# Kernel optimization log

Measured on AMD Instinct MI355X. Metric: run time of the kernel, lower is better.

Reference implementation:

```python
import jax, jax.numpy as jnp
import numpy as np

T, H, I = 4096, 4096, 11008  # tokens, hidden, intermediate


def setup_inputs() -> dict:
    key = jax.random.key(0)
    k = jax.random.split(key, 6)
    # int8-range quantized activations and weights (stored as int32 for jax matmul)
    x_q = jax.random.randint(k[0], (T, H), -127, 128).astype(jnp.int32)
    w_gate_up = jax.random.randint(k[1], (2 * I, H), -127, 128).astype(jnp.int32)
    w_down = jax.random.randint(k[2], (H, I), -127, 128).astype(jnp.int32)
    # per-token dynamic input scale, per-output-channel weight scales
    x_scale = jax.random.uniform(k[3], (T,), jnp.float32, 1e-4, 2e-2)
    s_w_gate_up = jax.random.uniform(k[4], (2 * I,), jnp.float32, 1e-4, 2e-2)
    s_w_down = jax.random.uniform(k[5], (H,), jnp.float32, 1e-4, 2e-2)
    return {"x_q": x_q, "x_scale": x_scale, "w_gate_up": w_gate_up,
            "s_w_gate_up": s_w_gate_up, "w_down": w_down, "s_w_down": s_w_down}


def reference(x_q, x_scale, w_gate_up, s_w_gate_up, w_down, s_w_down):
    # --- gate_up_proj: W8A8 int8 GEMM + dequant (per-token x per-channel scales) ---
    gu_i32 = jnp.matmul(x_q, w_gate_up.T)                                   # [T, 2I] int32 accum
    gu = gu_i32.astype(jnp.float32) * x_scale[:, None] * s_w_gate_up[None, :]
    gate, up = gu[:, :I], gu[:, I:]
    # --- SiluAndMulQuant: fused SiLU(gate)*up + per-token dynamic requant to int8 ---
    y = jax.nn.silu(gate) * up                                              # [T, I] fp
    s2 = jnp.maximum(jnp.max(jnp.abs(y), axis=-1), 1e-8) / 127.0            # [T] new dynamic scale
    y_q = jnp.clip(jnp.round(y / s2[:, None]), -128.0, 127.0).astype(jnp.int32)
    # --- down_proj: W8A8 int8 GEMM + dequant ---
    out_i32 = jnp.matmul(y_q, w_down.T)                                     # [T, H] int32 accum
    out = out_i32.astype(jnp.float32) * s2[:, None] * s_w_down[None, :]
    return out
```

## Files before the change

### kernel.cpp

```cpp
#include <hip/hip_runtime.h>
#include <cstdint>
#include <cstddef>

#define T_DIM 4096
#define H_DIM 4096
#define I_DIM 11008

typedef int v4i __attribute__((ext_vector_type(4)));

__device__ __forceinline__ void async_copy16(const void* g, void* l) {
  __builtin_amdgcn_global_load_lds(
      (const __attribute__((address_space(1))) void*)g,
      (__attribute__((address_space(3))) void*)l, 16, 0, 0);
}

__device__ __forceinline__ void stage_tile(const int8_t* src, size_t ld,
                                           char* ldsbase, int wave, int lane) {
#pragma unroll
  for (int q = 0; q < 2; ++q) {
    int seg = q * 4 + wave;
    int r = seg * 16 + (lane >> 2);
    int p = lane & 3;
    int c = p ^ ((r >> 1) & 3);
    const int8_t* g = src + (size_t)r * ld + (size_t)c * 16;
    char* lp = ldsbase + seg * 1024;
    async_copy16((const void*)g, (void*)lp);
  }
}

__device__ __forceinline__ v4i frag_load(const char* ldsbase, int rowbase, int lane) {
  int r = rowbase + (lane & 15);
  int c = (lane >> 4) ^ ((r >> 1) & 3);
  return *(const v4i*)(ldsbase + r * 64 + c * 16);
}

__global__ void pack_i8(const int4* __restrict__ src, char4* __restrict__ dst, int n4) {
  int stride = gridDim.x * blockDim.x;
  for (int i = blockIdx.x * blockDim.x + threadIdx.x; i < n4; i += stride) {
    int4 v = src[i];
    char4 c;
    c.x = (char)v.x; c.y = (char)v.y; c.z = (char)v.z; c.w = (char)v.w;
    dst[i] = c;
  }
}

__global__ void zero_u32(unsigned* __restrict__ p, int n) {
  int i = blockIdx.x * blockDim.x + threadIdx.x;
  if (i < n) p[i] = 0u;
}

__global__ __launch_bounds__(256, 2)
void gemm1_silu(const int8_t* __restrict__ x8,
                const int8_t* __restrict__ wgu8,
                const float* __restrict__ x_scale,
                const float* __restrict__ s_wgu,
                float* __restrict__ y,
                unsigned* __restrict__ rowmax) {
  __shared__ __align__(16) char lds[24 * 1024];
  char* ldsA  = lds;
  char* ldsBg = lds + 8192;
  char* ldsBu = lds + 16384;

  const int tid = threadIdx.x;
  const int wave = tid >> 6, lane = tid & 63;
  const int wm = wave >> 1, wn = wave & 1;
  const int m0 = blockIdx.y * 128;
  const int n0 = blockIdx.x * 128;

  v4i accg[4][4], accu[4][4];
  const v4i vzero = {0, 0, 0, 0};
#pragma unroll
  for (int i = 0; i < 4; i++)
#pragma unroll
    for (int j = 0; j < 4; j++) { accg[i][j] = vzero; accu[i][j] = vzero; }

  const int8_t* Ab  = x8 + (size_t)m0 * H_DIM;
  const int8_t* Bgb = wgu8 + (size_t)n0 * H_DIM;
  const int8_t* Bub = wgu8 + ((size_t)I_DIM + (size_t)n0) * H_DIM;

  for (int k0 = 0; k0 < H_DIM; k0 += 64) {
    __syncthreads();
    stage_tile(Ab + k0, H_DIM, ldsA, wave, lane);
    stage_tile(Bgb + k0, H_DIM, ldsBg, wave, lane);
    stage_tile(Bub + k0, H_DIM, ldsBu, wave, lane);
    __syncthreads();

    v4i a[4], bg[4], bu[4];
#pragma unroll
    for (int i = 0; i < 4; i++) a[i]  = frag_load(ldsA,  wm * 64 + i * 16, lane);
#pragma unroll
    for (int j = 0; j < 4; j++) bg[j] = frag_load(ldsBg, wn * 64 + j * 16, lane);
#pragma unroll
    for (int j = 0; j < 4; j++) bu[j] = frag_load(ldsBu, wn * 64 + j * 16, lane);

#pragma unroll
    for (int i = 0; i < 4; i++)
#pragma unroll
      for (int j = 0; j < 4; j++) {
        accg[i][j] = __builtin_amdgcn_mfma_i32_16x16x64_i8(a[i], bg[j], accg[i][j], 0, 0, 0);
        accu[i][j] = __builtin_amdgcn_mfma_i32_16x16x64_i8(a[i], bu[j], accu[i][j], 0, 0, 0);
      }
  }

  const int lr = lane >> 4;
  const int lc = lane & 15;
#pragma unroll
  for (int i = 0; i < 4; i++) {
#pragma unroll
    for (int t = 0; t < 4; t++) {
      const int gr = m0 + wm * 64 + i * 16 + lr * 4 + t;
      const float sx = x_scale[gr];
      float vmax = 0.f;
#pragma unroll
      for (int j = 0; j < 4; j++) {
        const int gc = n0 + wn * 64 + j * 16 + lc;
        float g = (float)accg[i][j][t] * sx * s_wgu[gc];
        float u = (float)accu[i][j][t] * sx * s_wgu[I_DIM + gc];
        float yv = (g / (1.f + expf(-g))) * u;
        y[(size_t)gr * I_DIM + gc] = yv;
        vmax = fmaxf(vmax, fabsf(yv));
      }
#pragma unroll
      for (int off = 1; off < 16; off <<= 1)
        vmax = fmaxf(vmax, __shfl_xor(vmax, off, 64));
      if (lc == 0) atomicMax(&rowmax[gr], __float_as_uint(vmax));
    }
  }
}

__global__ void quantize_y(const float* __restrict__ y,
                           const unsigned* __restrict__ rowmax,
                           int8_t* __restrict__ yq) {
  size_t gid = (size_t)blockIdx.x * blockDim.x + threadIdx.x;
  size_t base = gid * 4;
  if (base >= (size_t)T_DIM * I_DIM) return;
  int row = (int)(base / I_DIM);
  float inv = 127.f / fmaxf(__uint_as_float(rowmax[row]), 1e-8f);
  float4 v = *(const float4*)(y + base);
  char4 q;
  q.x = (char)(int)fminf(127.f, fmaxf(-128.f, rintf(v.x * inv)));
  q.y = (char)(int)fminf(127.f, fmaxf(-128.f, rintf(v.y * inv)));
  q.z = (char)(int)fminf(127.f, fmaxf(-128.f, rintf(v.z * inv)));
  q.w = (char)(int)fminf(127.f, fmaxf(-128.f, rintf(v.w * inv)));
  *(char4*)(yq + base) = q;
}

__global__ __launch_bounds__(256, 2)
void gemm2_scaled(const int8_t* __restrict__ yq8,
                  const int8_t* __restrict__ wd8,
                  const unsigned* __restrict__ rowmax,
                  const float* __restrict__ s_wd,
                  float* __restrict__ out) {
  __shared__ __align__(16) char lds[16 * 1024];
  char* ldsA = lds;
  char* ldsB = lds + 8192;

  const int tid = threadIdx.x;
  const int wave = tid >> 6, lane = tid & 63;
  const int wm = wave >> 1, wn = wave & 1;
  const int m0 = blockIdx.y * 128;
  const int n0 = blockIdx.x * 128;

  v4i acc[4][4];
  const v4i vzero = {0, 0, 0, 0};
#pragma unroll
  for (int i = 0; i < 4; i++)
#pragma unroll
    for (int j = 0; j < 4; j++) acc[i][j] = vzero;

  const int8_t* Ab = yq8 + (size_t)m0 * I_DIM;
  const int8_t* Bb = wd8 + (size_t)n0 * I_DIM;

  for (int k0 = 0; k0 < I_DIM; k0 += 64) {
    __syncthreads();
    stage_tile(Ab + k0, I_DIM, ldsA, wave, lane);
    stage_tile(Bb + k0, I_DIM, ldsB, wave, lane);
    __syncthreads();

    v4i a[4], b[4];
#pragma unroll
    for (int i = 0; i < 4; i++) a[i] = frag_load(ldsA, wm * 64 + i * 16, lane);
#pragma unroll
    for (int j = 0; j < 4; j++) b[j] = frag_load(ldsB, wn * 64 + j * 16, lane);

#pragma unroll
    for (int i = 0; i < 4; i++)
#pragma unroll
      for (int j = 0; j < 4; j++)
        acc[i][j] = __builtin_amdgcn_mfma_i32_16x16x64_i8(a[i], b[j], acc[i][j], 0, 0, 0);
  }

  const int lr = lane >> 4;
  const int lc = lane & 15;
#pragma unroll
  for (int i = 0; i < 4; i++) {
#pragma unroll
    for (int t = 0; t < 4; t++) {
      const int gr = m0 + wm * 64 + i * 16 + lr * 4 + t;
      const float s2 = fmaxf(__uint_as_float(rowmax[gr]), 1e-8f) / 127.f;
#pragma unroll
      for (int j = 0; j < 4; j++) {
        const int gc = n0 + wn * 64 + j * 16 + lc;
        out[(size_t)gr * H_DIM + gc] = (float)acc[i][j][t] * s2 * s_wd[gc];
      }
    }
  }
}

extern "C" void kernel_launch(void* const* d_in, const int* in_sizes, int n_in,
                              void* d_out, int out_size, void* d_ws, size_t ws_size,
                              hipStream_t stream) {
  const int*   x_q     = (const int*)d_in[0];
  const float* x_scale = (const float*)d_in[1];
  const int*   w_gu    = (const int*)d_in[2];
  const float* s_wgu   = (const float*)d_in[3];
  const int*   w_d     = (const int*)d_in[4];
  const float* s_wd    = (const float*)d_in[5];
  float* out = (float*)d_out;

  char* ws = (char*)d_ws;
  const size_t SZ_X8   = (size_t)T_DIM * H_DIM;
  const size_t SZ_WGU8 = (size_t)2 * I_DIM * H_DIM;
  const size_t SZ_WD8  = (size_t)H_DIM * I_DIM;
  const size_t SZ_Y    = (size_t)T_DIM * I_DIM * 4;
  const size_t SZ_YQ   = (size_t)T_DIM * I_DIM;

  int8_t*   x8     = (int8_t*)ws;
  int8_t*   wgu8   = (int8_t*)(ws + SZ_X8);
  int8_t*   wd8    = (int8_t*)(ws + SZ_X8 + SZ_WGU8);
  float*    y      = (float*)(ws + SZ_X8 + SZ_WGU8 + SZ_WD8);
  int8_t*   yq8    = (int8_t*)(ws + SZ_X8 + SZ_WGU8 + SZ_WD8 + SZ_Y);
  unsigned* rowmax = (unsigned*)(ws + SZ_X8 + SZ_WGU8 + SZ_WD8 + SZ_Y + SZ_YQ);

  pack_i8<<<dim3(8192), dim3(256), 0, stream>>>((const int4*)x_q,  (char4*)x8,   (int)(SZ_X8 / 4));
  pack_i8<<<dim3(8192), dim3(256), 0, stream>>>((const int4*)w_gu, (char4*)wgu8, (int)(SZ_WGU8 / 4));
  pack_i8<<<dim3(8192), dim3(256), 0, stream>>>((const int4*)w_d,  (char4*)wd8,  (int)(SZ_WD8 / 4));
  zero_u32<<<dim3(16), dim3(256), 0, stream>>>(rowmax, T_DIM);

  gemm1_silu<<<dim3(I_DIM / 128, T_DIM / 128), dim3(256), 0, stream>>>(
      x8, wgu8, x_scale, s_wgu, y, rowmax);

  quantize_y<<<dim3((unsigned)((size_t)T_DIM * I_DIM / 4 / 256)), dim3(256), 0, stream>>>(
      y, rowmax, yq8);

  gemm2_scaled<<<dim3(H_DIM / 128, T_DIM / 128), dim3(256), 0, stream>>>(
      yq8, wd8, rowmax, s_wd, out);
}
```

Baseline: 1.488 ms.

## Double-buffer LDS tiles and swizzle workgroup order in both int8 GEMMs

Both GEMM kernels now stage the next K tile into a second LDS buffer while MFMAs run on the current one. This removes one barrier per K step and overlaps global-to-LDS async copies with compute. Workgroup IDs are remapped with a stride-8 swizzle so that consecutive tiles land on the same XCD, which is meant to improve L2 reuse of A and B tiles. gemm2's launch bound also rises to 3 blocks per SIMD hint. In exchange, LDS use per block doubles, which could limit occupancy.

```diff
diff --git a/kernel.cpp b/kernel.cpp
--- a/kernel.cpp
+++ b/kernel.cpp
@@ -49,6 +49,25 @@
   if (i < n) p[i] = 0u;
 }
 
+__device__ __forceinline__ void g1_step(const char* LA, const char* LBG, const char* LBU,
+                                        int wm, int wn, int lane,
+                                        v4i (&accg)[4][4], v4i (&accu)[4][4]) {
+  v4i a[4], bg[4], bu[4];
+#pragma unroll
+  for (int i = 0; i < 4; i++) a[i]  = frag_load(LA,  wm * 64 + i * 16, lane);
+#pragma unroll
+  for (int j = 0; j < 4; j++) bg[j] = frag_load(LBG, wn * 64 + j * 16, lane);
+#pragma unroll
+  for (int j = 0; j < 4; j++) bu[j] = frag_load(LBU, wn * 64 + j * 16, lane);
+#pragma unroll
+  for (int i = 0; i < 4; i++)
+#pragma unroll
+    for (int j = 0; j < 4; j++) {
+      accg[i][j] = __builtin_amdgcn_mfma_i32_16x16x64_i8(a[i], bg[j], accg[i][j], 0, 0, 0);
+      accu[i][j] = __builtin_amdgcn_mfma_i32_16x16x64_i8(a[i], bu[j], accu[i][j], 0, 0, 0);
+    }
+}
+
 __global__ __launch_bounds__(256, 2)
 void gemm1_silu(const int8_t* __restrict__ x8,
                 const int8_t* __restrict__ wgu8,
@@ -56,16 +75,21 @@
                 const float* __restrict__ s_wgu,
                 float* __restrict__ y,
                 unsigned* __restrict__ rowmax) {
-  __shared__ __align__(16) char lds[24 * 1024];
-  char* ldsA  = lds;
-  char* ldsBg = lds + 8192;
-  char* ldsBu = lds + 16384;
+  __shared__ __align__(16) char lds0[24576];
+  __shared__ __align__(16) char lds1[24576];
+  char* A0 = lds0;  char* Bg0 = lds0 + 8192;  char* Bu0 = lds0 + 16384;
+  char* A1 = lds1;  char* Bg1 = lds1 + 8192;  char* Bu1 = lds1 + 16384;
 
   const int tid = threadIdx.x;
   const int wave = tid >> 6, lane = tid & 63;
   const int wm = wave >> 1, wn = wave & 1;
-  const int m0 = blockIdx.y * 128;
-  const int n0 = blockIdx.x * 128;
+
+  const unsigned nwg = gridDim.x * gridDim.y;
+  const unsigned bid = blockIdx.y * gridDim.x + blockIdx.x;
+  const unsigned cpx = nwg >> 3;
+  const unsigned swz = (bid & 7) * cpx + (bid >> 3);
+  const int m0 = (int)(swz / gridDim.x) * 128;
+  const int n0 = (int)(swz % gridDim.x) * 128;
 
   v4i accg[4][4], accu[4][4];
   const v4i vzero = {0, 0, 0, 0};
@@ -78,28 +102,32 @@
   const int8_t* Bgb = wgu8 + (size_t)n0 * H_DIM;
   const int8_t* Bub = wgu8 + ((size_t)I_DIM + (size_t)n0) * H_DIM;
 
-  for (int k0 = 0; k0 < H_DIM; k0 += 64) {
-    __syncthreads();
-    stage_tile(Ab + k0, H_DIM, ldsA, wave, lane);
-    stage_tile(Bgb + k0, H_DIM, ldsBg, wave, lane);
-    stage_tile(Bub + k0, H_DIM, ldsBu, wave, lane);
-    __syncthreads();
-
-    v4i a[4], bg[4], bu[4];
-#pragma unroll
-    for (int i = 0; i < 4; i++) a[i]  = frag_load(ldsA,  wm * 64 + i * 16, lane);
-#pragma unroll
-    for (int j = 0; j < 4; j++) bg[j] = frag_load(ldsBg, wn * 64 + j * 16, lane);
-#pragma unroll
-    for (int j = 0; j < 4; j++) bu[j] = frag_load(ldsBu, wn * 64 + j * 16, lane);
-
-#pragma unroll
-    for (int i = 0; i < 4; i++)
-#pragma unroll
-      for (int j = 0; j < 4; j++) {
-        accg[i][j] = __builtin_amdgcn_mfma_i32_16x16x64_i8(a[i], bg[j], accg[i][j], 0, 0, 0);
-        accu[i][j] = __builtin_amdgcn_mfma_i32_16x16x64_i8(a[i], bu[j], accu[i][j], 0, 0, 0);
-      }
+  stage_tile(Ab,  H_DIM, A0,  wave, lane);
+  stage_tile(Bgb, H_DIM, Bg0, wave, lane);
+  stage_tile(Bub, H_DIM, Bu0, wave, lane);
+  __syncthreads();
+
+  for (int k0 = 0; k0 < H_DIM; k0 += 128) {
+    {
+      const int kn = k0 + 64;
+      if (kn < H_DIM) {
+        stage_tile(Ab + kn,  H_DIM, A1,  wave, lane);
+        stage_tile(Bgb + kn, H_DIM, Bg1, wave, lane);
+        stage_tile(Bub + kn, H_DIM, Bu1, wave, lane);
+      }
+      g1_step(A0, Bg0, Bu0, wm, wn, lane, accg, accu);
+      __syncthreads();
+    }
+    {
+      const int kn = k0 + 128;
+      if (kn < H_DIM) {
+        stage_tile(Ab + kn,  H_DIM, A0,  wave, lane);
+        stage_tile(Bgb + kn, H_DIM, Bg0, wave, lane);
+        stage_tile(Bub + kn, H_DIM, Bu0, wave, lane);
+      }
+      g1_step(A1, Bg1, Bu1, wm, wn, lane, accg, accu);
+      __syncthreads();
+    }
   }
 
   const int lr = lane >> 4;
@@ -145,21 +173,42 @@
   *(char4*)(yq + base) = q;
 }
 
-__global__ __launch_bounds__(256, 2)
+__device__ __forceinline__ void g2_step(const char* LA, const char* LB,
+                                        int wm, int wn, int lane,
+                                        v4i (&acc)[4][4]) {
+  v4i a[4], b[4];
+#pragma unroll
+  for (int i = 0; i < 4; i++) a[i] = frag_load(LA, wm * 64 + i * 16, lane);
+#pragma unroll
+  for (int j = 0; j < 4; j++) b[j] = frag_load(LB, wn * 64 + j * 16, lane);
+#pragma unroll
+  for (int i = 0; i < 4; i++)
+#pragma unroll
+    for (int j = 0; j < 4; j++)
+      acc[i][j] = __builtin_amdgcn_mfma_i32_16x16x64_i8(a[i], b[j], acc[i][j], 0, 0, 0);
+}
+
+__global__ __launch_bounds__(256, 3)
 void gemm2_scaled(const int8_t* __restrict__ yq8,
                   const int8_t* __restrict__ wd8,
                   const unsigned* __restrict__ rowmax,
                   const float* __restrict__ s_wd,
                   float* __restrict__ out) {
-  __shared__ __align__(16) char lds[16 * 1024];
-  char* ldsA = lds;
-  char* ldsB = lds + 8192;
+  __shared__ __align__(16) char lds0[16384];
+  __shared__ __align__(16) char lds1[16384];
+  char* A0 = lds0;  char* B0 = lds0 + 8192;
+  char* A1 = lds1;  char* B1 = lds1 + 8192;
 
   const int tid = threadIdx.x;
   const int wave = tid >> 6, lane = tid & 63;
   const int wm = wave >> 1, wn = wave & 1;
-  const int m0 = blockIdx.y * 128;
-  const int n0 = blockIdx.x * 128;
+
+  const unsigned nwg = gridDim.x * gridDim.y;
+  const unsigned bid = blockIdx.y * gridDim.x + blockIdx.x;
+  const unsigned cpx = nwg >> 3;
+  const unsigned swz = (bid & 7) * cpx + (bid >> 3);
+  const int m0 = (int)(swz / gridDim.x) * 128;
+  const int n0 = (int)(swz % gridDim.x) * 128;
 
   v4i acc[4][4];
   const v4i vzero = {0, 0, 0, 0};
@@ -171,23 +220,29 @@
   const int8_t* Ab = yq8 + (size_t)m0 * I_DIM;
   const int8_t* Bb = wd8 + (size_t)n0 * I_DIM;
 
-  for (int k0 = 0; k0 < I_DIM; k0 += 64) {
-    __syncthreads();
-    stage_tile(Ab + k0, I_DIM, ldsA, wave, lane);
-    stage_tile(Bb + k0, I_DIM, ldsB, wave, lane);
-    __syncthreads();
-
-    v4i a[4], b[4];
-#pragma unroll
-    for (int i = 0; i < 4; i++) a[i] = frag_load(ldsA, wm * 64 + i * 16, lane);
-#pragma unroll
-    for (int j = 0; j < 4; j++) b[j] = frag_load(ldsB, wn * 64 + j * 16, lane);
-
-#pragma unroll
-    for (int i = 0; i < 4; i++)
-#pragma unroll
-      for (int j = 0; j < 4; j++)
-        acc[i][j] = __builtin_amdgcn_mfma_i32_16x16x64_i8(a[i], b[j], acc[i][j], 0, 0, 0);
+  stage_tile(Ab, I_DIM, A0, wave, lane);
+  stage_tile(Bb, I_DIM, B0, wave, lane);
+  __syncthreads();
+
+  for (int k0 = 0; k0 < I_DIM; k0 += 128) {
+    {
+      const int kn = k0 + 64;
+      if (kn < I_DIM) {
+        stage_tile(Ab + kn, I_DIM, A1, wave, lane);
+        stage_tile(Bb + kn, I_DIM, B1, wave, lane);
+      }
+      g2_step(A0, B0, wm, wn, lane, acc);
+      __syncthreads();
+    }
+    {
+      const int kn = k0 + 128;
+      if (kn < I_DIM) {
+        stage_tile(Ab + kn, I_DIM, A0, wave, lane);
+        stage_tile(Bb + kn, I_DIM, B0, wave, lane);
+      }
+      g2_step(A1, B1, wm, wn, lane, acc);
+      __syncthreads();
+    }
   }
 
   const int lr = lane >> 4;
```

Measured after the change: 1.475 ms. About the same (-0.8%).

## Triple-buffer LDS with async prefetch and XCD-aware tile swizzle in both GEMMs

Applied to the files above, without the earlier changes.

Both int8 GEMMs now use three LDS buffers, prefetching tiles two K-steps ahead with global_load_lds. Each step uses one vmcnt wait and one barrier instead of two __syncthreads, so global loads overlap MFMA work. Block indices are remapped so blocks that land on the same XCD share A rows, which should improve L2 reuse. LDS per block triples and gemm2 raises its occupancy hint to 3. The hand-counted vmcnt values and the unguarded final step depend on exact tile counts (64 and 172).

```diff
diff --git a/kernel.cpp b/kernel.cpp
--- a/kernel.cpp
+++ b/kernel.cpp
@@ -12,26 +12,6 @@
   __builtin_amdgcn_global_load_lds(
       (const __attribute__((address_space(1))) void*)g,
       (__attribute__((address_space(3))) void*)l, 16, 0, 0);
-}
-
-__device__ __forceinline__ void stage_tile(const int8_t* src, size_t ld,
-                                           char* ldsbase, int wave, int lane) {
-#pragma unroll
-  for (int q = 0; q < 2; ++q) {
-    int seg = q * 4 + wave;
-    int r = seg * 16 + (lane >> 2);
-    int p = lane & 3;
-    int c = p ^ ((r >> 1) & 3);
-    const int8_t* g = src + (size_t)r * ld + (size_t)c * 16;
-    char* lp = ldsbase + seg * 1024;
-    async_copy16((const void*)g, (void*)lp);
-  }
-}
-
-__device__ __forceinline__ v4i frag_load(const char* ldsbase, int rowbase, int lane) {
-  int r = rowbase + (lane & 15);
-  int c = (lane >> 4) ^ ((r >> 1) & 3);
-  return *(const v4i*)(ldsbase + r * 64 + c * 16);
 }
 
 __global__ void pack_i8(const int4* __restrict__ src, char4* __restrict__ dst, int n4) {
@@ -56,16 +36,21 @@
                 const float* __restrict__ s_wgu,
                 float* __restrict__ y,
                 unsigned* __restrict__ rowmax) {
-  __shared__ __align__(16) char lds[24 * 1024];
-  char* ldsA  = lds;
-  char* ldsBg = lds + 8192;
-  char* ldsBu = lds + 16384;
+  __shared__ __align__(16) char lds0[24576];
+  __shared__ __align__(16) char lds1[24576];
+  __shared__ __align__(16) char lds2[24576];
 
   const int tid = threadIdx.x;
   const int wave = tid >> 6, lane = tid & 63;
   const int wm = wave >> 1, wn = wave & 1;
-  const int m0 = blockIdx.y * 128;
-  const int n0 = blockIdx.x * 128;
+
+  const unsigned bid = blockIdx.y * gridDim.x + blockIdx.x;
+  const unsigned xcd = bid & 7;
+  const unsigned l   = bid >> 3;
+  const unsigned s   = l >> 5;
+  const unsigned r   = l - (s << 5);
+  const int m0 = (int)(xcd * 4 + (r & 3)) * 128;
+  const int n0 = (int)(s * 8 + (r >> 2)) * 128;
 
   v4i accg[4][4], accu[4][4];
   const v4i vzero = {0, 0, 0, 0};
@@ -78,29 +63,72 @@
   const int8_t* Bgb = wgu8 + (size_t)n0 * H_DIM;
   const int8_t* Bub = wgu8 + ((size_t)I_DIM + (size_t)n0) * H_DIM;
 
-  for (int k0 = 0; k0 < H_DIM; k0 += 64) {
-    __syncthreads();
-    stage_tile(Ab + k0, H_DIM, ldsA, wave, lane);
-    stage_tile(Bgb + k0, H_DIM, ldsBg, wave, lane);
-    stage_tile(Bub + k0, H_DIM, ldsBu, wave, lane);
-    __syncthreads();
-
-    v4i a[4], bg[4], bu[4];
-#pragma unroll
-    for (int i = 0; i < 4; i++) a[i]  = frag_load(ldsA,  wm * 64 + i * 16, lane);
-#pragma unroll
-    for (int j = 0; j < 4; j++) bg[j] = frag_load(ldsBg, wn * 64 + j * 16, lane);
-#pragma unroll
-    for (int j = 0; j < 4; j++) bu[j] = frag_load(ldsBu, wn * 64 + j * 16, lane);
-
-#pragma unroll
-    for (int i = 0; i < 4; i++)
-#pragma unroll
-      for (int j = 0; j < 4; j++) {
-        accg[i][j] = __builtin_amdgcn_mfma_i32_16x16x64_i8(a[i], bg[j], accg[i][j], 0, 0, 0);
-        accu[i][j] = __builtin_amdgcn_mfma_i32_16x16x64_i8(a[i], bu[j], accu[i][j], 0, 0, 0);
-      }
-  }
+  const int sr0 = wave * 16 + (lane >> 2);
+  const int sr1 = (4 + wave) * 16 + (lane >> 2);
+  const int sc0 = (lane & 3) ^ ((sr0 >> 1) & 3);
+  const int sc1 = (lane & 3) ^ ((sr1 >> 1) & 3);
+  const size_t vo0 = (size_t)sr0 * H_DIM + (size_t)sc0 * 16;
+  const size_t vo1 = (size_t)sr1 * H_DIM + (size_t)sc1 * 16;
+  const int ldsSeg0 = wave * 1024;
+  const int ldsSeg1 = (4 + wave) * 1024;
+
+  const int cfrag = ((lane >> 4) ^ (((lane & 15) >> 1) & 3)) * 16;
+  const int aoff = (wm * 64 + (lane & 15)) * 64 + cfrag;
+  const int boff = (wn * 64 + (lane & 15)) * 64 + cfrag;
+
+#define G1_STAGE(L, T)                                                      \
+  {                                                                         \
+    const int8_t* A_ = Ab + ((size_t)(T) << 6);                             \
+    const int8_t* G_ = Bgb + ((size_t)(T) << 6);                            \
+    const int8_t* U_ = Bub + ((size_t)(T) << 6);                            \
+    async_copy16(A_ + vo0, (L) + ldsSeg0);                                  \
+    async_copy16(A_ + vo1, (L) + ldsSeg1);                                  \
+    async_copy16(G_ + vo0, (L) + 8192 + ldsSeg0);                           \
+    async_copy16(G_ + vo1, (L) + 8192 + ldsSeg1);                           \
+    async_copy16(U_ + vo0, (L) + 16384 + ldsSeg0);                          \
+    async_copy16(U_ + vo1, (L) + 16384 + ldsSeg1);                          \
+  }
+
+#define G1_STEP(L)                                                          \
+  {                                                                         \
+    v4i a[4], bg[4], bu[4];                                                 \
+    _Pragma("unroll")                                                       \
+    for (int i = 0; i < 4; i++) a[i]  = *(const v4i*)((L) + aoff + i * 1024);          \
+    _Pragma("unroll")                                                       \
+    for (int j = 0; j < 4; j++) bg[j] = *(const v4i*)((L) + 8192 + boff + j * 1024);   \
+    _Pragma("unroll")                                                       \
+    for (int j = 0; j < 4; j++) bu[j] = *(const v4i*)((L) + 16384 + boff + j * 1024);  \
+    _Pragma("unroll")                                                       \
+    for (int i = 0; i < 4; i++)                                             \
+      _Pragma("unroll")                                                     \
+      for (int j = 0; j < 4; j++) {                                         \
+        accg[i][j] = __builtin_amdgcn_mfma_i32_16x16x64_i8(a[i], bg[j], accg[i][j], 0, 0, 0); \
+        accu[i][j] = __builtin_amdgcn_mfma_i32_16x16x64_i8(a[i], bu[j], accu[i][j], 0, 0, 0); \
+      }                                                                     \
+  }
+
+#define G1_PHASE(Lc, Ls, T)                                                 \
+  {                                                                         \
+    asm volatile("s_waitcnt vmcnt(6)" ::: "memory");                        \
+    __builtin_amdgcn_s_barrier();                                           \
+    if ((T) + 2 < 64) G1_STAGE(Ls, (T) + 2);                                \
+    G1_STEP(Lc);                                                            \
+  }
+
+  G1_STAGE(lds0, 0);
+  G1_STAGE(lds1, 1);
+
+  for (int t = 0; t < 63; t += 3) {
+    G1_PHASE(lds0, lds2, t)
+    G1_PHASE(lds1, lds0, t + 1)
+    G1_PHASE(lds2, lds1, t + 2)
+  }
+  asm volatile("s_waitcnt vmcnt(0)" ::: "memory");
+  __builtin_amdgcn_s_barrier();
+  G1_STEP(lds0);
+#undef G1_PHASE
+#undef G1_STEP
+#undef G1_STAGE
 
   const int lr = lane >> 4;
   const int lc = lane & 15;
@@ -145,21 +173,27 @@
   *(char4*)(yq + base) = q;
 }
 
-__global__ __launch_bounds__(256, 2)
+__global__ __launch_bounds__(256, 3)
 void gemm2_scaled(const int8_t* __restrict__ yq8,
                   const int8_t* __restrict__ wd8,
                   const unsigned* __restrict__ rowmax,
                   const float* __restrict__ s_wd,
                   float* __restrict__ out) {
-  __shared__ __align__(16) char lds[16 * 1024];
-  char* ldsA = lds;
-  char* ldsB = lds + 8192;
+  __shared__ __align__(16) char lds0[16384];
+  __shared__ __align__(16) char lds1[16384];
+  __shared__ __align__(16) char lds2[16384];
 
   const int tid = threadIdx.x;
   const int wave = tid >> 6, lane = tid & 63;
   const int wm = wave >> 1, wn = wave & 1;
-  const int m0 = blockIdx.y * 128;
-  const int n0 = blockIdx.x * 128;
+
+  const unsigned bid = blockIdx.y * gridDim.x + blockIdx.x;
+  const unsigned xcd = bid & 7;
+  const unsigned l   = bid >> 3;
+  const unsigned s   = l >> 5;
+  const unsigned r   = l & 31;
+  const int m0 = (int)(xcd * 4 + (r & 3)) * 128;
+  const int n0 = (int)(s * 8 + (r >> 2)) * 128;
 
   v4i acc[4][4];
   const v4i vzero = {0, 0, 0, 0};
@@ -171,24 +205,65 @@
   const int8_t* Ab = yq8 + (size_t)m0 * I_DIM;
   const int8_t* Bb = wd8 + (size_t)n0 * I_DIM;
 
-  for (int k0 = 0; k0 < I_DIM; k0 += 64) {
-    __syncthreads();
-    stage_tile(Ab + k0, I_DIM, ldsA, wave, lane);
-    stage_tile(Bb + k0, I_DIM, ldsB, wave, lane);
-    __syncthreads();
-
-    v4i a[4], b[4];
-#pragma unroll
-    for (int i = 0; i < 4; i++) a[i] = frag_load(ldsA, wm * 64 + i * 16, lane);
-#pragma unroll
-    for (int j = 0; j < 4; j++) b[j] = frag_load(ldsB, wn * 64 + j * 16, lane);
-
-#pragma unroll
-    for (int i = 0; i < 4; i++)
-#pragma unroll
-      for (int j = 0; j < 4; j++)
-        acc[i][j] = __builtin_amdgcn_mfma_i32_16x16x64_i8(a[i], b[j], acc[i][j], 0, 0, 0);
-  }
+  const int sr0 = wave * 16 + (lane >> 2);
+  const int sr1 = (4 + wave) * 16 + (lane >> 2);
+  const int sc0 = (lane & 3) ^ ((sr0 >> 1) & 3);
+  const int sc1 = (lane & 3) ^ ((sr1 >> 1) & 3);
+  const size_t vo0 = (size_t)sr0 * I_DIM + (size_t)sc0 * 16;
+  const size_t vo1 = (size_t)sr1 * I_DIM + (size_t)sc1 * 16;
+  const int ldsSeg0 = wave * 1024;
+  const int ldsSeg1 = (4 + wave) * 1024;
+
+  const int cfrag = ((lane >> 4) ^ (((lane & 15) >> 1) & 3)) * 16;
+  const int aoff = (wm * 64 + (lane & 15)) * 64 + cfrag;
+  const int boff = (wn * 64 + (lane & 15)) * 64 + cfrag;
+
+#define G2_STAGE(L, T)                                                      \
+  {                                                                         \
+    const int8_t* A_ = Ab + ((size_t)(T) << 6);                             \
+    const int8_t* B_ = Bb + ((size_t)(T) << 6);                             \
+    async_copy16(A_ + vo0, (L) + ldsSeg0);                                  \
+    async_copy16(A_ + vo1, (L) + ldsSeg1);                                  \
+    async_copy16(B_ + vo0, (L) + 8192 + ldsSeg0);                           \
+    async_copy16(B_ + vo1, (L) + 8192 + ldsSeg1);                           \
+  }
+
+#define G2_STEP(L)                                                          \
+  {                                                                         \
+    v4i a[4], b[4];                                                         \
+    _Pragma("unroll")                                                       \
+    for (int i = 0; i < 4; i++) a[i] = *(const v4i*)((L) + aoff + i * 1024);        \
+    _Pragma("unroll")                                                       \
+    for (int j = 0; j < 4; j++) b[j] = *(const v4i*)((L) + 8192 + boff + j * 1024); \
+    _Pragma("unroll")                                                       \
+    for (int i = 0; i < 4; i++)                                             \
+      _Pragma("unroll")                                                     \
+      for (int j = 0; j < 4; j++)                                           \
+        acc[i][j] = __builtin_amdgcn_mfma_i32_16x16x64_i8(a[i], b[j], acc[i][j], 0, 0, 0); \
+  }
+
+#define G2_PHASE(Lc, Ls, T)                                                 \
+  {                                                                         \
+    asm volatile("s_waitcnt vmcnt(4)" ::: "memory");                        \
+    __builtin_amdgcn_s_barrier();                                           \
+    if ((T) + 2 < 172) G2_STAGE(Ls, (T) + 2);                               \
+    G2_STEP(Lc);                                                            \
+  }
+
+  G2_STAGE(lds0, 0);
+  G2_STAGE(lds1, 1);
+
+  for (int t = 0; t < 171; t += 3) {
+    G2_PHASE(lds0, lds2, t)
+    G2_PHASE(lds1, lds0, t + 1)
+    G2_PHASE(lds2, lds1, t + 2)
+  }
+  asm volatile("s_waitcnt vmcnt(0)" ::: "memory");
+  __builtin_amdgcn_s_barrier();
+  G2_STEP(lds0);
+#undef G2_PHASE
+#undef G2_STEP
+#undef G2_STAGE
 
   const int lr = lane >> 4;
   const int lc = lane & 15;
```

New measurement: 1.381 ms. -7.2%, faster.
